# Kernel tuning notes

Measured on AMD Instinct MI355X. Metric: run time of the kernel, lower is better.

## Reference

```python
import jax, jax.numpy as jnp
import numpy as np

B = 131072
UNITS = 256
INPUT_DIM = 256


def setup_inputs() -> dict:
    key = jax.random.key(0)
    ks = jax.random.split(key, 8)
    x = jax.random.normal(ks[0], (B, INPUT_DIM), dtype=jnp.float32)
    h_prev = jax.random.normal(ks[1], (B, UNITS), dtype=jnp.float32)
    c_prev = jax.random.normal(ks[2], (B, UNITS), dtype=jnp.float32)
    # glorot-like scale for W: fan_in = INPUT_DIM + UNITS, fan_out = 4*UNITS
    scale = jnp.sqrt(2.0 / (INPUT_DIM + UNITS + 4 * UNITS)).astype(jnp.float32)
    W = jax.random.normal(ks[3], (INPUT_DIM + UNITS, 4 * UNITS), dtype=jnp.float32) * scale
    # bias: zeros except forget gate initialized to 1.0
    b = jnp.concatenate([
        jnp.zeros(UNITS, jnp.float32),
        jnp.ones(UNITS, jnp.float32),
        jnp.zeros(UNITS, jnp.float32),
        jnp.zeros(UNITS, jnp.float32),
    ])
    peephole_i = jax.random.normal(ks[4], (UNITS,), dtype=jnp.float32) * 0.05
    peephole_f = jax.random.normal(ks[5], (UNITS,), dtype=jnp.float32) * 0.05
    peephole_o = jax.random.normal(ks[6], (UNITS,), dtype=jnp.float32) * 0.05
    return {
        "x": x, "h_prev": h_prev, "c_prev": c_prev,
        "W": W, "b": b,
        "peephole_i": peephole_i, "peephole_f": peephole_f, "peephole_o": peephole_o,
    }


def reference(x, h_prev, c_prev, W, b, peephole_i, peephole_f, peephole_o):
    combined = jnp.concatenate([x, h_prev], axis=-1)          # [B, INPUT_DIM+UNITS]
    z = combined @ W + b                                      # [B, 4*UNITS]
    i, f, c_hat, o = jnp.split(z, 4, axis=1)                  # each [B, UNITS]
    i = jax.nn.sigmoid(i + peephole_i * c_prev)
    f = jax.nn.sigmoid(f + peephole_f * c_prev)
    o = jax.nn.sigmoid(o + peephole_o * c_prev)
    c_hat = jnp.tanh(c_hat)
    c = f * c_prev + i * c_hat
    h = o * jnp.tanh(c)
    return (h, h, c)  # matches (output, [h, c]) of the Keras cell
```

## Files before the change

### kernel.cpp

```cpp
#include <hip/hip_runtime.h>
#include <hip/hip_bf16.h>
#include <cstdint>

#define NROWS   131072
#define NUNITS  256
#define KTOT    512
#define BM      64
#define THREADS 512

typedef float f32x4  __attribute__((ext_vector_type(4)));
typedef short bf16x8 __attribute__((ext_vector_type(8)));

__device__ __forceinline__ short f2bf(float x) {
    unsigned u = __float_as_uint(x);
    u += 0x7FFFu + ((u >> 16) & 1u);
    return (short)(u >> 16);
}

#define BAR() do { asm volatile("s_waitcnt lgkmcnt(0)" ::: "memory"); \
                   __builtin_amdgcn_s_barrier(); } while (0)

__global__ void convert_W_kernel(const float* __restrict__ W, short* __restrict__ Wws) {
    int i = blockIdx.x * 256 + threadIdx.x;
    int k = i >> 10;
    int c = i & 1023;
    Wws[((size_t)(k >> 5) << 15) + ((size_t)c << 5) + (k & 31)] = f2bf(W[i]);
}

__global__ void __launch_bounds__(THREADS, 4)
lstm_main_kernel(const float* __restrict__ x, const float* __restrict__ h_prev,
                 const float* __restrict__ c_prev, const float* __restrict__ bias,
                 const float* __restrict__ pi, const float* __restrict__ pf,
                 const float* __restrict__ po, const short* __restrict__ Wws,
                 float* __restrict__ out) {
    __shared__ short Alds[2][BM * 32];

    const int bid = blockIdx.x;
    const int swz = (bid & 7) * 512 + (bid >> 3);
    const int rt  = swz >> 1;
    const int ch  = swz & 1;
    const int row0 = rt * BM;

    const int t    = threadIdx.x;
    const int lane = t & 63;
    const int w    = t >> 6;
    const int lr   = lane & 15;
    const int hi   = lane >> 4;

    const int srow  = t >> 3;
    const int sh    = t & 7;
    const int sg    = sh >> 1;
    const int shalf = sh & 1;
    const int s_lds = srow * 32 + ((sg ^ ((srow >> 1) & 3)) * 8) + shalf * 4;
    const float* aRowX = x      + (size_t)(row0 + srow) * 256 + sh * 4;
    const float* aRowH = h_prev + (size_t)(row0 + srow) * 256 + sh * 4;

    const int a_rd = lr * 32 + ((hi ^ ((lr >> 1) & 3)) * 8);

    const int ucol = ch * 128 + w * 16 + lr;
    const short* wbase = Wws + ((size_t)ucol << 5) + hi * 8;

    f32x4 acc[4][4];
    #pragma unroll
    for (int m = 0; m < 4; ++m)
        #pragma unroll
        for (int g = 0; g < 4; ++g)
            acc[m][g] = (f32x4){0.f, 0.f, 0.f, 0.f};

    bf16x8 Bcur[4], Bnext[4];

    auto loadA4 = [&](int kidx) -> float4 {
        return *(const float4*)((kidx < 8 ? aRowX : aRowH) + (kidx & 7) * 32);
    };
    auto writeA = [&](float4 av, int buf) {
        unsigned p0 = ((unsigned)(unsigned short)f2bf(av.y) << 16) | (unsigned short)f2bf(av.x);
        unsigned p1 = ((unsigned)(unsigned short)f2bf(av.w) << 16) | (unsigned short)f2bf(av.z);
        *(uint2*)(&Alds[buf][s_lds]) = make_uint2(p0, p1);
    };
    auto loadB = [&](int ks, bf16x8* B) {
        const short* wk = wbase + ((size_t)ks << 15);
        #pragma unroll
        for (int g = 0; g < 4; ++g)
            B[g] = *(const bf16x8*)(wk + g * 8192);
    };
    auto compute = [&](const bf16x8* B, int buf) {
        bf16x8 af[4];
        #pragma unroll
        for (int m = 0; m < 4; ++m)
            af[m] = *(const bf16x8*)&Alds[buf][a_rd + m * 16 * 32];
        #pragma unroll
        for (int g = 0; g < 4; ++g)
            #pragma unroll
            for (int m = 0; m < 4; ++m)
                acc[m][g] = __builtin_amdgcn_mfma_f32_16x16x32_bf16(af[m], B[g], acc[m][g], 0, 0, 0);
    };

    {
        float4 av0 = loadA4(0);
        loadB(0, Bcur);
        writeA(av0, 0);
        BAR();
    }

    #pragma unroll 1
    for (int it2 = 0; it2 < 7; ++it2) {
        const int k0 = 2 * it2;
        {
            float4 av = loadA4(k0 + 1);
            loadB(k0 + 1, Bnext);
            compute(Bcur, 0);
            writeA(av, 1);
            BAR();
        }
        {
            float4 av = loadA4(k0 + 2);
            loadB(k0 + 2, Bcur);
            compute(Bnext, 1);
            writeA(av, 0);
            BAR();
        }
    }
    {
        float4 av = loadA4(15);
        loadB(15, Bnext);
        compute(Bcur, 0);
        writeA(av, 1);
        BAR();
        compute(Bnext, 1);
    }

    const size_t HS = (size_t)NROWS * NUNITS;
    const int u = ucol;
    const float bi = bias[u],       bfg = bias[256 + u];
    const float bc = bias[512 + u], bo  = bias[768 + u];
    const float ppi = pi[u], ppf = pf[u], ppo = po[u];
    #pragma unroll
    for (int m = 0; m < 4; ++m) {
        #pragma unroll
        for (int r = 0; r < 4; ++r) {
            const int row = row0 + m * 16 + hi * 4 + r;
            const size_t o = (size_t)row * NUNITS + u;
            const float cp = c_prev[o];
            float zi = acc[m][0][r] + bi  + ppi * cp;
            float zf = acc[m][1][r] + bfg + ppf * cp;
            float zc = acc[m][2][r] + bc;
            float zo = acc[m][3][r] + bo  + ppo * cp;
            float ig = 1.f / (1.f + __expf(-zi));
            float fg = 1.f / (1.f + __expf(-zf));
            float og = 1.f / (1.f + __expf(-zo));
            zc = fminf(fmaxf(zc, -30.f), 30.f);
            float e2 = __expf(2.f * zc);
            float chat = (e2 - 1.f) / (e2 + 1.f);
            float c  = fg * cp + ig * chat;
            float ccl = fminf(fmaxf(c, -30.f), 30.f);
            float e3 = __expf(2.f * ccl);
            float th = (e3 - 1.f) / (e3 + 1.f);
            float h  = og * th;
            out[o]          = h;
            out[HS + o]     = h;
            out[2 * HS + o] = c;
        }
    }
}

extern "C" void kernel_launch(void* const* d_in, const int* in_sizes, int n_in,
                              void* d_out, int out_size, void* d_ws, size_t ws_size,
                              hipStream_t stream) {
    const float* x  = (const float*)d_in[0];
    const float* h  = (const float*)d_in[1];
    const float* c  = (const float*)d_in[2];
    const float* W  = (const float*)d_in[3];
    const float* b  = (const float*)d_in[4];
    const float* pi = (const float*)d_in[5];
    const float* pf = (const float*)d_in[6];
    const float* po = (const float*)d_in[7];
    short* Wws = (short*)d_ws;
    float* out = (float*)d_out;

    hipLaunchKernelGGL(convert_W_kernel, dim3(2048), dim3(256), 0, stream, W, Wws);
    hipLaunchKernelGGL(lstm_main_kernel, dim3(2 * NROWS / BM), dim3(THREADS), 0, stream,
                       x, h, c, b, pi, pf, po, Wws, out);
}
```

Measured before the change: 347.6 us.

## Widen A LDS stage to 64-wide K and deepen A/B prefetch pipeline

Doubles the K-depth per LDS stage (64 instead of 32), so each thread loads 8 floats per row segment and writes one 16-byte packed bf16 store. This halves the number of barriers. It also prefetches A two stages ahead and rotates three B register sets to hide global latency. The occupancy hint drops from 4 to 3 blocks per CU to give room for the extra registers, which may reduce latency hiding from concurrent waves.

```diff
diff --git a/kernel.cpp b/kernel.cpp
--- a/kernel.cpp
+++ b/kernel.cpp
@@ -16,6 +16,9 @@
     u += 0x7FFFu + ((u >> 16) & 1u);
     return (short)(u >> 16);
 }
+__device__ __forceinline__ unsigned pack2(float lo, float hi) {
+    return ((unsigned)(unsigned short)f2bf(hi) << 16) | (unsigned short)f2bf(lo);
+}
 
 #define BAR() do { asm volatile("s_waitcnt lgkmcnt(0)" ::: "memory"); \
                    __builtin_amdgcn_s_barrier(); } while (0)
@@ -27,13 +30,13 @@
     Wws[((size_t)(k >> 5) << 15) + ((size_t)c << 5) + (k & 31)] = f2bf(W[i]);
 }
 
-__global__ void __launch_bounds__(THREADS, 4)
+__global__ void __launch_bounds__(THREADS, 3)
 lstm_main_kernel(const float* __restrict__ x, const float* __restrict__ h_prev,
                  const float* __restrict__ c_prev, const float* __restrict__ bias,
                  const float* __restrict__ pi, const float* __restrict__ pf,
                  const float* __restrict__ po, const short* __restrict__ Wws,
                  float* __restrict__ out) {
-    __shared__ short Alds[2][BM * 32];
+    __shared__ short Alds[2][BM * 64];
 
     const int bid = blockIdx.x;
     const int swz = (bid & 7) * 512 + (bid >> 3);
@@ -47,15 +50,11 @@
     const int lr   = lane & 15;
     const int hi   = lane >> 4;
 
-    const int srow  = t >> 3;
-    const int sh    = t & 7;
-    const int sg    = sh >> 1;
-    const int shalf = sh & 1;
-    const int s_lds = srow * 32 + ((sg ^ ((srow >> 1) & 3)) * 8) + shalf * 4;
-    const float* aRowX = x      + (size_t)(row0 + srow) * 256 + sh * 4;
-    const float* aRowH = h_prev + (size_t)(row0 + srow) * 256 + sh * 4;
-
-    const int a_rd = lr * 32 + ((hi ^ ((lr >> 1) & 3)) * 8);
+    const int srow = t >> 3;
+    const int sg   = t & 7;
+    const int s_lds = srow * 64 + ((sg ^ (srow & 7)) * 8);
+    const float* aRowX = x      + (size_t)(row0 + srow) * 256 + sg * 8;
+    const float* aRowH = h_prev + (size_t)(row0 + srow) * 256 + sg * 8;
 
     const int ucol = ch * 128 + w * 16 + lr;
     const short* wbase = Wws + ((size_t)ucol << 5) + hi * 8;
@@ -67,27 +66,34 @@
         for (int g = 0; g < 4; ++g)
             acc[m][g] = (f32x4){0.f, 0.f, 0.f, 0.f};
 
-    bf16x8 Bcur[4], Bnext[4];
+    bf16x8 BA[4], BB[4], BC[4];
+    float4 sE[2], sO[2];
 
-    auto loadA4 = [&](int kidx) -> float4 {
-        return *(const float4*)((kidx < 8 ? aRowX : aRowH) + (kidx & 7) * 32);
-    };
-    auto writeA = [&](float4 av, int buf) {
-        unsigned p0 = ((unsigned)(unsigned short)f2bf(av.y) << 16) | (unsigned short)f2bf(av.x);
-        unsigned p1 = ((unsigned)(unsigned short)f2bf(av.w) << 16) | (unsigned short)f2bf(av.z);
-        *(uint2*)(&Alds[buf][s_lds]) = make_uint2(p0, p1);
-    };
-    auto loadB = [&](int ks, bf16x8* B) {
+    auto loadBset = [&](int ks, bf16x8* B) {
         const short* wk = wbase + ((size_t)ks << 15);
         #pragma unroll
         for (int g = 0; g < 4; ++g)
             B[g] = *(const bf16x8*)(wk + g * 8192);
     };
-    auto compute = [&](const bf16x8* B, int buf) {
+    auto loadA2 = [&](int p, float4* s) {
+        const float* base = (p < 4 ? aRowX : aRowH) + (p & 3) * 64;
+        s[0] = *(const float4*)base;
+        s[1] = *(const float4*)(base + 4);
+    };
+    auto writeA = [&](const float4* s, int buf) {
+        int4 v;
+        v.x = pack2(s[0].x, s[0].y);
+        v.y = pack2(s[0].z, s[0].w);
+        v.z = pack2(s[1].x, s[1].y);
+        v.w = pack2(s[1].z, s[1].w);
+        *(int4*)&Alds[buf][s_lds] = v;
+    };
+    auto mfmaHalf = [&](const bf16x8* B, int buf, int kk) {
         bf16x8 af[4];
         #pragma unroll
         for (int m = 0; m < 4; ++m)
-            af[m] = *(const bf16x8*)&Alds[buf][a_rd + m * 16 * 32];
+            af[m] = *(const bf16x8*)&Alds[buf][(m * 16 + lr) * 64
+                                              + (((kk * 4 + hi) ^ (lr & 7)) * 8)];
         #pragma unroll
         for (int g = 0; g < 4; ++g)
             #pragma unroll
@@ -95,38 +101,36 @@
                 acc[m][g] = __builtin_amdgcn_mfma_f32_16x16x32_bf16(af[m], B[g], acc[m][g], 0, 0, 0);
     };
 
-    {
-        float4 av0 = loadA4(0);
-        loadB(0, Bcur);
-        writeA(av0, 0);
-        BAR();
-    }
+    loadA2(0, sE);
+    loadA2(1, sO);
+    loadBset(0, BA);
+    writeA(sE, 0);
+    BAR();
 
     #pragma unroll 1
-    for (int it2 = 0; it2 < 7; ++it2) {
-        const int k0 = 2 * it2;
+    for (int p2 = 0; p2 < 4; ++p2) {
+        const int pe = 2 * p2;
         {
-            float4 av = loadA4(k0 + 1);
-            loadB(k0 + 1, Bnext);
-            compute(Bcur, 0);
-            writeA(av, 1);
+            loadBset(2 * pe + 1, BB);
+            if (pe < 7) loadBset(2 * pe + 2, BC);
+            if (pe < 6) loadA2(pe + 2, sE);
+            mfmaHalf(BA, 0, 0);
+            mfmaHalf(BB, 0, 1);
+            writeA(sO, 1);
             BAR();
         }
+        const int po = pe + 1;
         {
-            float4 av = loadA4(k0 + 2);
-            loadB(k0 + 2, Bcur);
-            compute(Bnext, 1);
-            writeA(av, 0);
-            BAR();
+            loadBset(2 * po + 1, BB);
+            if (po < 7) loadBset(2 * po + 2, BA);
+            if (po < 6) loadA2(po + 2, sO);
+            mfmaHalf(BC, 1, 0);
+            mfmaHalf(BB, 1, 1);
+            if (po < 7) {
+                writeA(sE, 0);
+                BAR();
+            }
         }
-    }
-    {
-        float4 av = loadA4(15);
-        loadB(15, Bnext);
-        compute(Bcur, 0);
-        writeA(av, 1);
-        BAR();
-        compute(Bnext, 1);
     }
 
     const size_t HS = (size_t)NROWS * NUNITS;
```

Result: slower. 397.5 us (+14.4%).
